# Kernel optimization log

Hardware: AMD Instinct MI355X
Metric: run time of the kernel (lower is better)

Reference implementation:

```python
import jax, jax.numpy as jnp
import numpy as np

B, A, M = 8, 200_000, 64


def calc_iou(a, b):
    # a: [A,4] anchors, b: [M,4] gt boxes (x1,y1,x2,y2)
    area_b = (b[:, 2] - b[:, 0]) * (b[:, 3] - b[:, 1])            # [M]
    iw = jnp.clip(jnp.minimum(a[:, 2:3], b[:, 2]) - jnp.maximum(a[:, 0:1], b[:, 0]), 0.0)
    ih = jnp.clip(jnp.minimum(a[:, 3:4], b[:, 3]) - jnp.maximum(a[:, 1:2], b[:, 1]), 0.0)
    area_a = ((a[:, 2] - a[:, 0]) * (a[:, 3] - a[:, 1]))[:, None]  # [A,1]
    inter = iw * ih                                                # [A,M]
    ua = jnp.clip(area_a + area_b - inter, 1e-8)
    return inter / ua


def setup_inputs() -> dict:
    key = jax.random.key(0)
    k1, k2, k3, k4, k5, k6, k7, k8 = jax.random.split(key, 8)
    classifications = jax.random.normal(k1, (B, A, 2), dtype=jnp.float32)
    bbox_regressions = jax.random.normal(k2, (B, A, 4), dtype=jnp.float32) * 0.1
    # realistic anchor boxes over a 640x640 image
    cx = jax.random.uniform(k3, (A,), minval=0.0, maxval=640.0)
    cy = jax.random.uniform(k4, (A,), minval=0.0, maxval=640.0)
    wh = jax.random.uniform(k5, (A, 2), minval=8.0, maxval=128.0)
    anchor = jnp.stack([cx - wh[:, 0] / 2, cy - wh[:, 1] / 2,
                        cx + wh[:, 0] / 2, cy + wh[:, 1] / 2], axis=1)
    anchors = anchor[None]  # [1,A,4]
    # GT boxes sampled near anchors so positives (IoU>=0.5) actually occur
    idx = jax.random.randint(k6, (B, M), 0, A)
    ann = anchor[idx] + jax.random.normal(k7, (B, M, 4)) * 1.5
    invalid = jax.random.uniform(k8, (B, M)) < 0.25
    x1 = jnp.where(invalid, -1.0, jnp.maximum(ann[..., 0], 0.5))
    ann = ann.at[..., 0].set(x1)
    return {"classifications": classifications, "bbox_regressions": bbox_regressions,
            "anchors": anchors, "annotations": ann.astype(jnp.float32)}


BOX_STD = jnp.array([0.1, 0.1, 0.2, 0.2], dtype=jnp.float32)


def _forward(classifications, bbox_regressions, anchors, annotations):
    anchor = anchors[0]
    aw = anchor[:, 2] - anchor[:, 0]
    ah = anchor[:, 3] - anchor[:, 1]
    acx = anchor[:, 0] + 0.5 * aw
    acy = anchor[:, 1] + 0.5 * ah
    ar = jnp.arange(A)

    def per_image(cls, reg, ann):
        valid = ann[:, 0] > 0                      # [M] (torch filters these rows out)
        boxes = ann[:, :4]
        iou = calc_iou(anchor, boxes)              # [A,M]
        iou = jnp.where(valid[None, :], iou, -1.0)  # invalid GT never matched
        iou_max = jnp.max(iou, axis=1)
        iou_arg = jnp.argmax(iou, axis=1)
        pos = iou_max >= 0.5
        neg = iou_max < 0.3
        num_pos = jnp.sum(pos)
        num_neg = jnp.sum(neg)
        keep = num_pos * 3
        eff = jnp.minimum(keep, num_neg)           # torch truncates sorted losses to keep
        # hard negative mining: sort -cls[:,1] over negatives, descending
        neg_l = jnp.where(neg, -cls[:, 1], -jnp.inf)
        sorted_neg = -jnp.sort(-neg_l)             # descending, -inf last
        sel = ar < eff
        efff = jnp.maximum(eff, 1).astype(cls.dtype)
        neg_mean = jnp.sum(jnp.where(sel, sorted_neg, 0.0)) / efff
        nposf = jnp.maximum(num_pos, 1).astype(cls.dtype)
        pos_mean = jnp.sum(jnp.where(pos, -cls[:, 0], 0.0)) / nposf
        cls_loss = jnp.where(num_pos > 0, pos_mean + neg_mean, 0.0)
        ag = boxes[iou_arg]                        # [A,4] assigned GT per anchor
        gw = ag[:, 2] - ag[:, 0]
        gh = ag[:, 3] - ag[:, 1]
        gcx = ag[:, 0] + 0.5 * gw
        gcy = ag[:, 1] + 0.5 * gh
        dx = (gcx - acx) / (aw + 1e-14)
        dy = (gcy - acy) / (ah + 1e-14)
        dw = jnp.log(jnp.where(pos, gw / aw, 1.0))  # guard log for non-positive rows
        dh = jnp.log(jnp.where(pos, gh / ah, 1.0))
        targets = jnp.stack([dx, dy, dw, dh], axis=1) / BOX_STD  # [A,4]
        d = jnp.abs(targets - reg)
        sl = jnp.where(d < 1.0, 0.5 * d * d, d - 0.5)  # SmoothL1, beta=1
        denom = jnp.maximum(num_pos * 4, 1).astype(cls.dtype)
        box_loss = jnp.sum(jnp.where(pos[:, None], sl, 0.0)) / denom
        box_loss = jnp.where(num_pos > 0, box_loss, 0.0)
        return cls_loss, box_loss

    cls_losses, box_losses = jax.vmap(per_image)(classifications, bbox_regressions, annotations)
    return cls_losses, box_losses


def reference(classifications, bbox_regressions, anchors, annotations):
    return _forward(classifications, bbox_regressions, anchors, annotations)
```

## Files before the change

### kernel.cpp

```cpp
#include <hip/hip_runtime.h>
#include <stdint.h>

#define NA 200000
#define NB 8
#define NM 64
#define APB 1024
#define CPB 196
#define NA4 50000
#define SPB 128
#define SEGCAP 25600
#define IMGCAP (8*SEGCAP)

#define O_SCAL 0
#define O_L1C  128
#define O_L1S  2176
#define O_KEYS 4224
#define O_CBUF 1604224
#define N_ZERO 4224

__device__ __forceinline__ unsigned int f2key(float f) {
    unsigned int u = __float_as_uint(f);
    return (u & 0x80000000u) ? ~u : (u | 0x80000000u);
}
__device__ __forceinline__ float key2f(unsigned int k) {
    return (k & 0x80000000u) ? __uint_as_float(k & 0x7fffffffu) : __uint_as_float(~k);
}
__device__ __forceinline__ unsigned int calck(const unsigned int* scal, int b) {
    const unsigned int np = scal[b * 16], nn = scal[b * 16 + 1];
    if (!np) return 0u;
    const unsigned int kp = np * 3u;
    return (kp < nn) ? kp : nn;
}

__device__ __forceinline__ void wave_sel256(
    const unsigned int* __restrict__ cnt, const float* __restrict__ sum,
    unsigned int target, unsigned int* c, unsigned int* cab, float* sab)
{
    const int lane = (int)(threadIdx.x & 63u);
    const uint4  c4 = ((const uint4*)cnt)[lane];
    const float4 s4 = ((const float4*)sum)[lane];
    unsigned int S = c4.x + c4.y + c4.z + c4.w;
    float Sf = s4.x + s4.y + s4.z + s4.w;
    for (int d = 1; d < 64; d <<= 1) {
        const unsigned int oc = __shfl_down(S, d);
        const float of = __shfl_down(Sf, d);
        if (lane + d < 64) { S += oc; Sf += of; }
    }
    unsigned int Sn = __shfl_down(S, 1);
    float Sfn = __shfl_down(Sf, 1);
    if (lane == 63) { Sn = 0u; Sfn = 0.0f; }
    const unsigned int cb[4] = {c4.x, c4.y, c4.z, c4.w};
    const float sb[4] = {s4.x, s4.y, s4.z, s4.w};
    unsigned int run = Sn; float runs = Sfn;
    bool found = false; unsigned int lc = 0, lcab = 0; float lsab = 0.0f;
#pragma unroll
    for (int j = 3; j >= 0; --j) {
        const unsigned int prev = run; const float prevs = runs;
        run += cb[j]; runs += sb[j];
        if (run >= target && prev < target) {
            found = true; lc = (unsigned int)(4 * lane + j); lcab = prev; lsab = prevs;
        }
    }
    const unsigned long long m = __ballot(found);
    const int src = __ffsll((long long)m) - 1;
    *c = __shfl(lc, src); *cab = __shfl(lcab, src); *sab = __shfl(lsab, src);
}

__device__ __forceinline__ void wave_sel4096_cnt(
    const unsigned int* hc, unsigned int target, unsigned int* bin, unsigned int* cab)
{
    const int lane = (int)(threadIdx.x & 63u);
    unsigned int cs = 0;
    const uint4* p = (const uint4*)(hc + lane * 64);
#pragma unroll
    for (int j = 0; j < 16; ++j) { const uint4 u = p[j]; cs += u.x + u.y + u.z + u.w; }
    unsigned int S = cs;
    for (int d = 1; d < 64; d <<= 1) { const unsigned int o = __shfl_down(S, d); if (lane + d < 64) S += o; }
    unsigned int Sn = __shfl_down(S, 1); if (lane == 63) Sn = 0u;
    const bool f1 = (S >= target) && (Sn < target);
    const unsigned long long m1 = __ballot(f1);
    const int chunk = __ffsll((long long)m1) - 1;
    const unsigned int above = __shfl(Sn, chunk);
    unsigned int S2 = hc[chunk * 64 + lane];
    for (int d = 1; d < 64; d <<= 1) { const unsigned int o = __shfl_down(S2, d); if (lane + d < 64) S2 += o; }
    unsigned int S2n = __shfl_down(S2, 1); if (lane == 63) S2n = 0u;
    const bool f2 = (above + S2 >= target) && (above + S2n < target);
    const unsigned long long m2 = __ballot(f2);
    const int l2 = __ffsll((long long)m2) - 1;
    *bin = (unsigned int)(chunk * 64 + l2);
    *cab = above + __shfl(S2n, l2);
}

__device__ __forceinline__ void iou_upd(
    const float4 Aq, const float aaq, const float4 B, const float abj, const int j,
    float& bi, float& bu, int& arg)
{
#pragma clang fp contract(off)
    const float iw = fmaxf(fminf(Aq.z, B.z) - fmaxf(Aq.x, B.x), 0.0f);
    const float ih = fmaxf(fminf(Aq.w, B.w) - fmaxf(Aq.y, B.y), 0.0f);
    const float inter = iw * ih;
    const float ua = fmaxf(aaq + abj - inter, 1e-8f);
    if (inter * bu > bi * ua) { bi = inter; bu = ua; arg = j; }
}

__device__ __forceinline__ void epi2(
    int b, int i, float4 a4, int arg, bool pos, bool neg, float2 cv,
    const float* __restrict__ reg, const float4* sbox, unsigned int* __restrict__ keys,
    unsigned int* hc8, float* hs8, float& posv, float& boxv)
{
    unsigned int key = 0u;
    if (neg) {
        const float nl = -cv.y;
        key = f2key(nl);
        atomicAdd(&hc8[key >> 24], 1u);
        atomicAdd(&hs8[key >> 24], nl);
    }
    keys[(size_t)b * NA + i] = key;
    if (pos) {
        posv += -cv.x;
        const float4 g = sbox[arg];
        const float aw = a4.z - a4.x, ah = a4.w - a4.y;
        const float acx = a4.x + 0.5f * aw, acy = a4.y + 0.5f * ah;
        const float gw = g.z - g.x, gh = g.w - g.y;
        const float gcx = g.x + 0.5f * gw, gcy = g.y + 0.5f * gh;
        const float t0 = ((gcx - acx) / (aw + 1e-14f)) / 0.1f;
        const float t1 = ((gcy - acy) / (ah + 1e-14f)) / 0.1f;
        const float t2 = logf(gw / aw) / 0.2f;
        const float t3 = logf(gh / ah) / 0.2f;
        const float4 r = ((const float4*)reg)[(size_t)b * NA + i];
        const float d0 = fabsf(t0 - r.x);
        const float d1 = fabsf(t1 - r.y);
        const float d2 = fabsf(t2 - r.z);
        const float d3 = fabsf(t3 - r.w);
        const float l0 = (d0 < 1.0f) ? 0.5f * d0 * d0 : d0 - 0.5f;
        const float l1 = (d1 < 1.0f) ? 0.5f * d1 * d1 : d1 - 0.5f;
        const float l2 = (d2 < 1.0f) ? 0.5f * d2 * d2 : d2 - 0.5f;
        const float l3 = (d3 < 1.0f) ? 0.5f * d3 * d3 : d3 - 0.5f;
        boxv += l0 + l1 + l2 + l3;
    }
}

__global__ __launch_bounds__(256, 4) void k_main(
    const float* __restrict__ cls, const float* __restrict__ reg,
    const float* __restrict__ anchors, const float* __restrict__ ann,
    unsigned int* __restrict__ scal, unsigned int* __restrict__ l1cnt,
    float* __restrict__ l1sum, unsigned int* __restrict__ keys)
{
    __shared__ float4 sbox[NM];
    __shared__ unsigned int s_nv;
    __shared__ unsigned int hc8[256];
    __shared__ float hs8[256];
    __shared__ unsigned int s_np, s_nn;
    __shared__ float s_ps, s_bs;

    const int b = blockIdx.y;
    const int tid = threadIdx.x;
    const int ibase = blockIdx.x * APB + tid;

    float4 A[4]; float2 CV[4];
#pragma unroll
    for (int q = 0; q < 4; ++q) {
        const int i = ibase + q * 256;
        if (i < NA) {
            A[q]  = ((const float4*)anchors)[i];
            CV[q] = ((const float2*)cls)[(size_t)b * NA + i];
        } else {
            A[q]  = make_float4(0.f, 0.f, 0.f, 0.f);
            CV[q] = make_float2(0.f, 0.f);
        }
    }

    if (tid < NM) {
        const float4 bb = ((const float4*)ann)[b * NM + tid];
        const bool valid = (bb.x > 0.0f);
        const unsigned long long m = __ballot(valid);
        if (valid) {
            const int p = __popcll(m & ((1ull << (tid & 63)) - 1ull));
            sbox[p] = bb;
        }
        if (tid == 0) s_nv = (unsigned int)__popcll(m);
    }
    hc8[tid] = 0u; hs8[tid] = 0.0f;
    if (tid == 0) { s_np = 0u; s_nn = 0u; s_ps = 0.0f; s_bs = 0.0f; }
    __syncthreads();
    const int nv = (int)s_nv;
    const int nvr = (nv + 3) & ~3;
    if (tid >= nv && tid < nvr) {
        sbox[tid] = make_float4(__builtin_inff(), __builtin_inff(),
                                -__builtin_inff(), -__builtin_inff());
    }
    __syncthreads();

    float aa[4];
    {
#pragma clang fp contract(off)
#pragma unroll
        for (int q = 0; q < 4; ++q) aa[q] = (A[q].z - A[q].x) * (A[q].w - A[q].y);
    }
    float bi[4] = {-1.0f, -1.0f, -1.0f, -1.0f};
    float bu[4] = {1.0f, 1.0f, 1.0f, 1.0f};
    int arg[4] = {0, 0, 0, 0};

#pragma unroll 1
    for (int mo = 0; mo < nvr; mo += 4) {
        const float4 b0 = sbox[mo + 0];
        const float4 b1 = sbox[mo + 1];
        const float4 b2 = sbox[mo + 2];
        const float4 b3 = sbox[mo + 3];
        float ab0, ab1, ab2, ab3;
        {
#pragma clang fp contract(off)
            ab0 = (b0.z - b0.x) * (b0.w - b0.y);
            ab1 = (b1.z - b1.x) * (b1.w - b1.y);
            ab2 = (b2.z - b2.x) * (b2.w - b2.y);
            ab3 = (b3.z - b3.x) * (b3.w - b3.y);
        }
#pragma unroll
        for (int q = 0; q < 4; ++q) {
            iou_upd(A[q], aa[q], b0, ab0, mo + 0, bi[q], bu[q], arg[q]);
            iou_upd(A[q], aa[q], b1, ab1, mo + 1, bi[q], bu[q], arg[q]);
            iou_upd(A[q], aa[q], b2, ab2, mo + 2, bi[q], bu[q], arg[q]);
            iou_upd(A[q], aa[q], b3, ab3, mo + 3, bi[q], bu[q], arg[q]);
        }
    }

    bool pos[4], neg[4];
    {
#pragma clang fp contract(off)
#pragma unroll
        for (int q = 0; q < 4; ++q) {
            pos[q] = (bi[q] >= 0.5f * bu[q]);
            neg[q] = (bi[q] < 0.3f * bu[q]);
        }
    }

    float posv = 0.0f, boxv = 0.0f;
#pragma unroll
    for (int q = 0; q < 4; ++q) {
        const int i = ibase + q * 256;
        if (i < NA) {
            epi2(b, i, A[q], arg[q], pos[q], neg[q], CV[q], reg, sbox, keys, hc8, hs8, posv, boxv);
        } else { pos[q] = false; neg[q] = false; }
    }

    unsigned int pc = 0, nc = 0; bool anyp = false;
#pragma unroll
    for (int q = 0; q < 4; ++q) {
        const unsigned long long pb = __ballot(pos[q]);
        const unsigned long long nb = __ballot(neg[q]);
        anyp |= (pb != 0ull);
        pc += (unsigned int)__popcll(pb);
        nc += (unsigned int)__popcll(nb);
    }
    if (anyp) {
        for (int off = 32; off; off >>= 1) {
            posv += __shfl_xor(posv, off);
            boxv += __shfl_xor(boxv, off);
        }
    }
    if ((tid & 63) == 0) {
        if (nc) atomicAdd(&s_nn, nc);
        if (pc) { atomicAdd(&s_np, pc); atomicAdd(&s_ps, posv); atomicAdd(&s_bs, boxv); }
    }
    __syncthreads();
    unsigned int* sg = scal + b * 16;
    if (tid == 0) {
        if (s_nn) atomicAdd(&sg[1], s_nn);
        if (s_np) {
            atomicAdd(&sg[0], s_np);
            atomicAdd((float*)(sg + 2), s_ps);
            atomicAdd((float*)(sg + 3), s_bs);
        }
    }
    if (hc8[tid]) {
        atomicAdd(&l1cnt[b * 256 + tid], hc8[tid]);
        atomicAdd(&l1sum[b * 256 + tid], hs8[tid]);
    }
}

__global__ __launch_bounds__(256) void k_h2c(
    const unsigned int* __restrict__ keys, unsigned int* __restrict__ scal,
    const unsigned int* __restrict__ l1c, const float* __restrict__ l1s,
    unsigned int* __restrict__ cbuf)
{
    __shared__ unsigned int wcnt[4];
    __shared__ unsigned int sbase;
    const int b = blockIdx.x >> 7;
    const int sub = blockIdx.x & (SPB - 1);
    const int tid = threadIdx.x;
    const unsigned int k = calck(scal, b);
    if (k == 0) return;
    unsigned int c1, cab1; float sab1;
    wave_sel256(l1c + b * 256, l1s + b * 256, k, &c1, &cab1, &sab1);

    const uint4* kp4 = (const uint4*)(keys + (size_t)b * NA);
    const int j0 = sub * 256 + tid;
    const int j1 = j0 + SPB * 256;
    const uint4 v0 = kp4[j0];
    const uint4 v1 = (j1 < NA4) ? kp4[j1] : make_uint4(0, 0, 0, 0);
    const unsigned int kk[8] = {v0.x, v0.y, v0.z, v0.w, v1.x, v1.y, v1.z, v1.w};

    const int lane = tid & 63;
    const int wave = tid >> 6;
    bool m[8];
    unsigned long long mask[8];
    unsigned int tot = 0;
#pragma unroll
    for (int j = 0; j < 8; ++j) {
        m[j] = kk[j] && (kk[j] >> 24) == c1;
        mask[j] = __ballot(m[j]);
        tot += (unsigned int)__popcll(mask[j]);
    }
    if (lane == 0) wcnt[wave] = tot;
    __syncthreads();
    if (tid == 0) {
        unsigned int p = 0;
#pragma unroll
        for (int w = 0; w < 4; ++w) { const unsigned int t = wcnt[w]; wcnt[w] = p; p += t; }
        sbase = p ? atomicAdd(&scal[b * 16 + 8 + (sub & 7)], p) : 0u;
    }
    __syncthreads();
    unsigned int base = sbase + wcnt[wave];
    if (tot) {
        unsigned int* cb = cbuf + (size_t)b * IMGCAP + (sub & 7) * SEGCAP;
        const unsigned long long lt = (lane == 63) ? ~0ull >> 1 : ((1ull << (lane + 1)) - 1ull) >> 1;
#pragma unroll
        for (int j = 0; j < 8; ++j) {
            if (m[j]) cb[base + (unsigned int)__popcll(mask[j] & lt)] = kk[j];
            base += (unsigned int)__popcll(mask[j]);
        }
    }
}

__global__ __launch_bounds__(1024) void k_fin2(
    const unsigned int* __restrict__ scal,
    const unsigned int* __restrict__ l1c, const float* __restrict__ l1s,
    const unsigned int* __restrict__ cbuf, float* __restrict__ out)
{
    __shared__ unsigned int hc[4096];
    __shared__ unsigned int s_sel[2];
    __shared__ float spart[16];

    const int b = blockIdx.x;
    const int tid = threadIdx.x;
    const unsigned int np = scal[b * 16];
    const unsigned int k = calck(scal, b);
    float s_top = 0.0f;

    if (k > 0) {
        unsigned int c1, cab1; float sab1;
        wave_sel256(l1c + b * 256, l1s + b * 256, k, &c1, &cab1, &sab1);
        const unsigned int t2 = k - cab1;
        unsigned int ns[8];
#pragma unroll
        for (int s = 0; s < 8; ++s) ns[s] = scal[b * 16 + 8 + s];

        for (int j = tid; j < 4096; j += 1024) hc[j] = 0u;
        __syncthreads();
#pragma unroll 1
        for (int s = 0; s < 8; ++s) {
            const unsigned int n2 = ns[s];
            const unsigned int* cb = cbuf + (size_t)b * IMGCAP + s * SEGCAP;
            for (unsigned int base = 0; base < n2; base += 4096) {
                const unsigned int i0 = base + tid, i1 = i0 + 1024, i2 = i0 + 2048, i3 = i0 + 3072;
                const unsigned int k0 = (i0 < n2) ? cb[i0] : 0u;
                const unsigned int k1 = (i1 < n2) ? cb[i1] : 0u;
                const unsigned int k2 = (i2 < n2) ? cb[i2] : 0u;
                const unsigned int k3 = (i3 < n2) ? cb[i3] : 0u;
                if (i0 < n2) atomicAdd(&hc[(k0 >> 12) & 0xfffu], 1u);
                if (i1 < n2) atomicAdd(&hc[(k1 >> 12) & 0xfffu], 1u);
                if (i2 < n2) atomicAdd(&hc[(k2 >> 12) & 0xfffu], 1u);
                if (i3 < n2) atomicAdd(&hc[(k3 >> 12) & 0xfffu], 1u);
            }
        }
        __syncthreads();
        if (tid < 64) {
            unsigned int c2w, cab2w;
            wave_sel4096_cnt(hc, t2, &c2w, &cab2w);
            if (tid == 0) { s_sel[0] = c2w; s_sel[1] = cab2w; }
        }
        __syncthreads();
        const unsigned int c2 = s_sel[0];
        const unsigned int t3 = t2 - s_sel[1];
        __syncthreads();

        for (int j = tid; j < 4096; j += 1024) hc[j] = 0u;
        __syncthreads();
#pragma unroll 1
        for (int s = 0; s < 8; ++s) {
            const unsigned int n2 = ns[s];
            const unsigned int* cb = cbuf + (size_t)b * IMGCAP + s * SEGCAP;
            for (unsigned int base = 0; base < n2; base += 4096) {
                const unsigned int i0 = base + tid, i1 = i0 + 1024, i2 = i0 + 2048, i3 = i0 + 3072;
                const unsigned int k0 = (i0 < n2) ? cb[i0] : 0u;
                const unsigned int k1 = (i1 < n2) ? cb[i1] : 0u;
                const unsigned int k2 = (i2 < n2) ? cb[i2] : 0u;
                const unsigned int k3 = (i3 < n2) ? cb[i3] : 0u;
                if (i0 < n2 && ((k0 >> 12) & 0xfffu) == c2) atomicAdd(&hc[k0 & 0xfffu], 1u);
                if (i1 < n2 && ((k1 >> 12) & 0xfffu) == c2) atomicAdd(&hc[k1 & 0xfffu], 1u);
                if (i2 < n2 && ((k2 >> 12) & 0xfffu) == c2) atomicAdd(&hc[k2 & 0xfffu], 1u);
                if (i3 < n2 && ((k3 >> 12) & 0xfffu) == c2) atomicAdd(&hc[k3 & 0xfffu], 1u);
            }
        }
        __syncthreads();
        if (tid < 64) {
            unsigned int c3w, cab3w;
            wave_sel4096_cnt(hc, t3, &c3w, &cab3w);
            if (tid == 0) { s_sel[0] = c3w; s_sel[1] = cab3w; }
        }
        __syncthreads();
        const unsigned int keyv = (c1 << 24) | (c2 << 12) | s_sel[0];
        const unsigned int rem = t3 - s_sel[1];
        const float v = key2f(keyv);

        float ls = 0.0f;
#pragma unroll 1
        for (int s = 0; s < 8; ++s) {
            const unsigned int n2 = ns[s];
            const unsigned int* cb = cbuf + (size_t)b * IMGCAP + s * SEGCAP;
            for (unsigned int base = 0; base < n2; base += 4096) {
                const unsigned int i0 = base + tid, i1 = i0 + 1024, i2 = i0 + 2048, i3 = i0 + 3072;
                const unsigned int k0 = (i0 < n2) ? cb[i0] : 0u;
                const unsigned int k1 = (i1 < n2) ? cb[i1] : 0u;
                const unsigned int k2 = (i2 < n2) ? cb[i2] : 0u;
                const unsigned int k3 = (i3 < n2) ? cb[i3] : 0u;
                if (k0 > keyv) ls += key2f(k0);
                if (k1 > keyv) ls += key2f(k1);
                if (k2 > keyv) ls += key2f(k2);
                if (k3 > keyv) ls += key2f(k3);
            }
        }
        for (int off = 32; off; off >>= 1) ls += __shfl_xor(ls, off);
        if ((tid & 63) == 0) spart[tid >> 6] = ls;
        __syncthreads();
        if (tid == 0) {
            float S = 0.0f;
#pragma unroll
            for (int w = 0; w < 16; ++w) S += spart[w];
            s_top = sab1 + S + (float)rem * v;
        }
    }

    if (tid == 0) {
        float cls_loss = 0.0f, box_loss = 0.0f;
        if (np > 0) {
            const float* fsc = (const float*)(scal + b * 16);
            const float pos_mean = fsc[2] / (float)np;
            const float neg_mean = s_top / (float)((k > 0) ? k : 1u);
            cls_loss = pos_mean + neg_mean;
            box_loss = fsc[3] / (float)(4u * np);
        }
        out[b] = cls_loss;
        out[NB + b] = box_loss;
    }
}

extern "C" void kernel_launch(void* const* d_in, const int* in_sizes, int n_in,
                              void* d_out, int out_size, void* d_ws, size_t ws_size,
                              hipStream_t stream) {
    const float* cls     = (const float*)d_in[0];
    const float* reg     = (const float*)d_in[1];
    const float* anchors = (const float*)d_in[2];
    const float* ann     = (const float*)d_in[3];
    unsigned int* ws = (unsigned int*)d_ws;
    unsigned int* scal = ws + O_SCAL;
    unsigned int* l1c  = ws + O_L1C;   float* l1s = (float*)(ws + O_L1S);
    unsigned int* keys = ws + O_KEYS;
    unsigned int* cbuf = ws + O_CBUF;
    (void)in_sizes; (void)n_in; (void)out_size; (void)ws_size;

    hipMemsetAsync(d_ws, 0, (size_t)N_ZERO * 4, stream);
    k_main<<<dim3(CPB, NB),  256,  0, stream>>>(cls, reg, anchors, ann, scal, l1c, l1s, keys);
    k_h2c <<<dim3(NB * SPB), 256,  0, stream>>>(keys, scal, l1c, l1s, cbuf);
    k_fin2<<<dim3(NB),       1024, 0, stream>>>(scal, l1c, l1s, cbuf, (float*)d_out);
}
```

Measured before the change: 173.8 us.

## Build second-level histogram during compaction and cache third-level candidates in LDS

Level-2 radix histogram counts are accumulated in global memory with atomics inside k_h2c while candidates are compacted, so k_fin2 no longer rescans the compacted buffer to build that histogram. The level-3 histogram pass is merged with the partial-sum pass: keys above the level-2 bin are summed directly and keys in the bin are staged into an LDS array, which is then scanned for the final tail sum. This cuts k_fin2's three passes over the candidate buffer to one, at the cost of global atomics in k_h2c, a larger memset, extra LDS, and a fallback rescan if the staged bin overflows.

```diff
diff --git a/kernel.cpp b/kernel.cpp
--- a/kernel.cpp
+++ b/kernel.cpp
@@ -10,13 +10,15 @@
 #define SPB 128
 #define SEGCAP 25600
 #define IMGCAP (8*SEGCAP)
+#define C2CAP 6144
 
 #define O_SCAL 0
 #define O_L1C  128
 #define O_L1S  2176
-#define O_KEYS 4224
-#define O_CBUF 1604224
-#define N_ZERO 4224
+#define O_GH4K 4224
+#define O_KEYS 36992
+#define O_CBUF 1636992
+#define N_ZERO 36992
 
 __device__ __forceinline__ unsigned int f2key(float f) {
     unsigned int u = __float_as_uint(f);
@@ -281,7 +283,7 @@
 __global__ __launch_bounds__(256) void k_h2c(
     const unsigned int* __restrict__ keys, unsigned int* __restrict__ scal,
     const unsigned int* __restrict__ l1c, const float* __restrict__ l1s,
-    unsigned int* __restrict__ cbuf)
+    unsigned int* __restrict__ cbuf, unsigned int* __restrict__ gh4k)
 {
     __shared__ unsigned int wcnt[4];
     __shared__ unsigned int sbase;
@@ -300,6 +302,7 @@
     const uint4 v1 = (j1 < NA4) ? kp4[j1] : make_uint4(0, 0, 0, 0);
     const unsigned int kk[8] = {v0.x, v0.y, v0.z, v0.w, v1.x, v1.y, v1.z, v1.w};
 
+    unsigned int* gh = gh4k + b * 4096;
     const int lane = tid & 63;
     const int wave = tid >> 6;
     bool m[8];
@@ -310,6 +313,7 @@
         m[j] = kk[j] && (kk[j] >> 24) == c1;
         mask[j] = __ballot(m[j]);
         tot += (unsigned int)__popcll(mask[j]);
+        if (m[j]) atomicAdd(&gh[(kk[j] >> 12) & 0xfffu], 1u);
     }
     if (lane == 0) wcnt[wave] = tot;
     __syncthreads();
@@ -335,11 +339,14 @@
 __global__ __launch_bounds__(1024) void k_fin2(
     const unsigned int* __restrict__ scal,
     const unsigned int* __restrict__ l1c, const float* __restrict__ l1s,
-    const unsigned int* __restrict__ cbuf, float* __restrict__ out)
+    const unsigned int* __restrict__ cbuf, const unsigned int* __restrict__ gh4k,
+    float* __restrict__ out)
 {
     __shared__ unsigned int hc[4096];
     __shared__ unsigned int s_sel[2];
     __shared__ float spart[16];
+    __shared__ unsigned int s_cnt;
+    __shared__ unsigned int cbin[C2CAP];
 
     const int b = blockIdx.x;
     const int tid = threadIdx.x;
@@ -355,24 +362,8 @@
 #pragma unroll
         for (int s = 0; s < 8; ++s) ns[s] = scal[b * 16 + 8 + s];
 
-        for (int j = tid; j < 4096; j += 1024) hc[j] = 0u;
-        __syncthreads();
-#pragma unroll 1
-        for (int s = 0; s < 8; ++s) {
-            const unsigned int n2 = ns[s];
-            const unsigned int* cb = cbuf + (size_t)b * IMGCAP + s * SEGCAP;
-            for (unsigned int base = 0; base < n2; base += 4096) {
-                const unsigned int i0 = base + tid, i1 = i0 + 1024, i2 = i0 + 2048, i3 = i0 + 3072;
-                const unsigned int k0 = (i0 < n2) ? cb[i0] : 0u;
-                const unsigned int k1 = (i1 < n2) ? cb[i1] : 0u;
-                const unsigned int k2 = (i2 < n2) ? cb[i2] : 0u;
-                const unsigned int k3 = (i3 < n2) ? cb[i3] : 0u;
-                if (i0 < n2) atomicAdd(&hc[(k0 >> 12) & 0xfffu], 1u);
-                if (i1 < n2) atomicAdd(&hc[(k1 >> 12) & 0xfffu], 1u);
-                if (i2 < n2) atomicAdd(&hc[(k2 >> 12) & 0xfffu], 1u);
-                if (i3 < n2) atomicAdd(&hc[(k3 >> 12) & 0xfffu], 1u);
-            }
-        }
+        for (int j = tid; j < 4096; j += 1024) hc[j] = gh4k[b * 4096 + j];
+        if (tid == 0) s_cnt = 0u;
         __syncthreads();
         if (tid < 64) {
             unsigned int c2w, cab2w;
@@ -382,36 +373,8 @@
         __syncthreads();
         const unsigned int c2 = s_sel[0];
         const unsigned int t3 = t2 - s_sel[1];
-        __syncthreads();
-
         for (int j = tid; j < 4096; j += 1024) hc[j] = 0u;
         __syncthreads();
-#pragma unroll 1
-        for (int s = 0; s < 8; ++s) {
-            const unsigned int n2 = ns[s];
-            const unsigned int* cb = cbuf + (size_t)b * IMGCAP + s * SEGCAP;
-            for (unsigned int base = 0; base < n2; base += 4096) {
-                const unsigned int i0 = base + tid, i1 = i0 + 1024, i2 = i0 + 2048, i3 = i0 + 3072;
-                const unsigned int k0 = (i0 < n2) ? cb[i0] : 0u;
-                const unsigned int k1 = (i1 < n2) ? cb[i1] : 0u;
-                const unsigned int k2 = (i2 < n2) ? cb[i2] : 0u;
-                const unsigned int k3 = (i3 < n2) ? cb[i3] : 0u;
-                if (i0 < n2 && ((k0 >> 12) & 0xfffu) == c2) atomicAdd(&hc[k0 & 0xfffu], 1u);
-                if (i1 < n2 && ((k1 >> 12) & 0xfffu) == c2) atomicAdd(&hc[k1 & 0xfffu], 1u);
-                if (i2 < n2 && ((k2 >> 12) & 0xfffu) == c2) atomicAdd(&hc[k2 & 0xfffu], 1u);
-                if (i3 < n2 && ((k3 >> 12) & 0xfffu) == c2) atomicAdd(&hc[k3 & 0xfffu], 1u);
-            }
-        }
-        __syncthreads();
-        if (tid < 64) {
-            unsigned int c3w, cab3w;
-            wave_sel4096_cnt(hc, t3, &c3w, &cab3w);
-            if (tid == 0) { s_sel[0] = c3w; s_sel[1] = cab3w; }
-        }
-        __syncthreads();
-        const unsigned int keyv = (c1 << 24) | (c2 << 12) | s_sel[0];
-        const unsigned int rem = t3 - s_sel[1];
-        const float v = key2f(keyv);
 
         float ls = 0.0f;
 #pragma unroll 1
@@ -424,12 +387,57 @@
                 const unsigned int k1 = (i1 < n2) ? cb[i1] : 0u;
                 const unsigned int k2 = (i2 < n2) ? cb[i2] : 0u;
                 const unsigned int k3 = (i3 < n2) ? cb[i3] : 0u;
-                if (k0 > keyv) ls += key2f(k0);
-                if (k1 > keyv) ls += key2f(k1);
-                if (k2 > keyv) ls += key2f(k2);
-                if (k3 > keyv) ls += key2f(k3);
+                const unsigned int kk4[4] = {k0, k1, k2, k3};
+#pragma unroll
+                for (int j = 0; j < 4; ++j) {
+                    const unsigned int kj = kk4[j];
+                    const unsigned int mid = (kj >> 12) & 0xfffu;
+                    if (mid > c2) ls += key2f(kj);
+                    else if (kj && mid == c2) {
+                        const unsigned int idx = atomicAdd(&s_cnt, 1u);
+                        if (idx < C2CAP) cbin[idx] = kj;
+                        atomicAdd(&hc[kj & 0xfffu], 1u);
+                    }
+                }
             }
         }
+        __syncthreads();
+        if (tid < 64) {
+            unsigned int c3w, cab3w;
+            wave_sel4096_cnt(hc, t3, &c3w, &cab3w);
+            if (tid == 0) { s_sel[0] = c3w; s_sel[1] = cab3w; }
+        }
+        __syncthreads();
+        const unsigned int c3 = s_sel[0];
+        const unsigned int keyv = (c1 << 24) | (c2 << 12) | c3;
+        const unsigned int rem = t3 - s_sel[1];
+        const float v = key2f(keyv);
+        const unsigned int cnt2 = s_cnt;
+
+        if (cnt2 <= C2CAP) {
+            for (unsigned int i = tid; i < cnt2; i += 1024) {
+                const unsigned int kj = cbin[i];
+                if ((kj & 0xfffu) > c3) ls += key2f(kj);
+            }
+        } else {
+#pragma unroll 1
+            for (int s = 0; s < 8; ++s) {
+                const unsigned int n2 = ns[s];
+                const unsigned int* cb = cbuf + (size_t)b * IMGCAP + s * SEGCAP;
+                for (unsigned int base = 0; base < n2; base += 4096) {
+                    const unsigned int i0 = base + tid, i1 = i0 + 1024, i2 = i0 + 2048, i3 = i0 + 3072;
+                    const unsigned int k0 = (i0 < n2) ? cb[i0] : 0u;
+                    const unsigned int k1 = (i1 < n2) ? cb[i1] : 0u;
+                    const unsigned int k2 = (i2 < n2) ? cb[i2] : 0u;
+                    const unsigned int k3 = (i3 < n2) ? cb[i3] : 0u;
+                    if (k0 && ((k0 >> 12) & 0xfffu) == c2 && (k0 & 0xfffu) > c3) ls += key2f(k0);
+                    if (k1 && ((k1 >> 12) & 0xfffu) == c2 && (k1 & 0xfffu) > c3) ls += key2f(k1);
+                    if (k2 && ((k2 >> 12) & 0xfffu) == c2 && (k2 & 0xfffu) > c3) ls += key2f(k2);
+                    if (k3 && ((k3 >> 12) & 0xfffu) == c2 && (k3 & 0xfffu) > c3) ls += key2f(k3);
+                }
+            }
+        }
+
         for (int off = 32; off; off >>= 1) ls += __shfl_xor(ls, off);
         if ((tid & 63) == 0) spart[tid >> 6] = ls;
         __syncthreads();
@@ -465,12 +473,13 @@
     unsigned int* ws = (unsigned int*)d_ws;
     unsigned int* scal = ws + O_SCAL;
     unsigned int* l1c  = ws + O_L1C;   float* l1s = (float*)(ws + O_L1S);
+    unsigned int* gh4k = ws + O_GH4K;
     unsigned int* keys = ws + O_KEYS;
     unsigned int* cbuf = ws + O_CBUF;
     (void)in_sizes; (void)n_in; (void)out_size; (void)ws_size;
 
     hipMemsetAsync(d_ws, 0, (size_t)N_ZERO * 4, stream);
     k_main<<<dim3(CPB, NB),  256,  0, stream>>>(cls, reg, anchors, ann, scal, l1c, l1s, keys);
-    k_h2c <<<dim3(NB * SPB), 256,  0, stream>>>(keys, scal, l1c, l1s, cbuf);
-    k_fin2<<<dim3(NB),       1024, 0, stream>>>(scal, l1c, l1s, cbuf, (float*)d_out);
-}
+    k_h2c <<<dim3(NB * SPB), 256,  0, stream>>>(keys, scal, l1c, l1s, cbuf, gh4k);
+    k_fin2<<<dim3(NB),       1024, 0, stream>>>(scal, l1c, l1s, cbuf, gh4k, (float*)d_out);
+}
```

Measured after the change: 178.3 us. +2.6%, slower.
